# Optimization experiments

Measured on AMD Instinct MI355X. Metric: run time of the kernel, lower is better.

## Reference

```python
import jax, jax.numpy as jnp
import numpy as np

RADIUS = 0.3
NSAMPLE = 16
NPOINT = 256
EPS = 1e-5


def setup_inputs() -> dict:
    key = jax.random.key(0)
    ks = jax.random.split(key, 12)
    B, N, C = 16, 16384, 288
    d = {
        "xyz": jax.random.uniform(ks[0], (B, N, 3), jnp.float32),
        "features": jax.random.normal(ks[1], (B, C, N), jnp.float32),
    }
    cin = [C + 3, C, C]  # use_xyz adds 3 to first SharedMLP width
    for i in range(3):
        d[f"W{i}"] = jax.random.normal(ks[2 + i], (C, cin[i]), jnp.float32) / np.float32(np.sqrt(cin[i]))
        d[f"g{i}"] = jnp.ones((C,), jnp.float32)
        d[f"b{i}"] = jnp.zeros((C,), jnp.float32)
        d[f"m{i}"] = jax.random.normal(ks[5 + i], (C,), jnp.float32) * 0.1
        d[f"v{i}"] = jax.random.uniform(ks[8 + i], (C,), jnp.float32, minval=0.5, maxval=1.5)
    return d


def fps(xyz, npoint):
    """Farthest point sampling. xyz: (B,N,3) -> inds (B,npoint) int32."""
    B, N, _ = xyz.shape
    d0 = jnp.full((B, N), 1e10, xyz.dtype)
    i0 = jnp.zeros((B,), jnp.int32)  # CUDA kernel starts from index 0

    def step(carry, _):
        dist, idx = carry
        cur = jnp.take_along_axis(xyz, idx[:, None, None], axis=1)  # (B,1,3)
        d = jnp.sum((xyz - cur) ** 2, axis=-1)  # (B,N)
        dist = jnp.minimum(dist, d)
        nxt = jnp.argmax(dist, axis=-1).astype(jnp.int32)
        return (dist, nxt), idx

    _, inds = jax.lax.scan(step, (d0, i0), None, length=npoint)
    return inds.T  # (B, npoint)


def ball_query(xyz, new_xyz):
    """xyz: (B,N,3), new_xyz: (B,S,3) -> idx (B,S,NSAMPLE) int32.
    First NSAMPLE in-radius indices; pad with the first found index (CUDA semantics)."""
    N = xyz.shape[1]
    d2 = jnp.sum((new_xyz[:, :, None, :] - xyz[:, None, :, :]) ** 2, axis=-1)  # (B,S,N)
    mask = d2 < RADIUS * RADIUS
    cand = jnp.where(mask, jnp.arange(N, dtype=jnp.int32), jnp.int32(N))
    cand = jnp.sort(cand, axis=-1)[..., :NSAMPLE]
    first = cand[..., :1]
    return jnp.where(cand == N, first, cand)


def _mlp_bn_relu(h, W, g, b, m, v):
    # 1x1 Conv2d (no bias) + BatchNorm (running stats) + ReLU on (B,C,S,K)
    h = jnp.einsum('oc,bcsk->bosk', W, h)
    scale = (g * jax.lax.rsqrt(v + EPS))[:, None, None]
    return jax.nn.relu((h - m[:, None, None]) * scale + b[:, None, None])


def reference(xyz, features, W0, g0, b0, m0, v0, W1, g1, b1, m1, v1, W2, g2, b2, m2, v2):
    inds = fps(xyz, NPOINT)                                   # (B,S)
    new_xyz = jax.vmap(lambda p, i: p[i])(xyz, inds)          # (B,S,3)
    idx = ball_query(xyz, new_xyz)                            # (B,S,K)
    g_xyz = jax.vmap(lambda p, i: p[i])(xyz, idx)             # (B,S,K,3)
    g_xyz = (g_xyz - new_xyz[:, :, None, :]) / RADIUS         # normalize_xyz
    g_feat = jax.vmap(lambda f, i: f[:, i])(features, idx)    # (B,C,S,K)
    h = jnp.concatenate([jnp.transpose(g_xyz, (0, 3, 1, 2)), g_feat], axis=1)  # (B,C+3,S,K)
    for (W, g, b, m, v) in ((W0, g0, b0, m0, v0), (W1, g1, b1, m1, v1), (W2, g2, b2, m2, v2)):
        h = _mlp_bn_relu(h, W, g, b, m, v)
    new_features = jnp.max(h, axis=-1)                        # (B,C,S) max-pool over nsample
    return new_xyz, new_features, inds
```

## Files before the change

kernel.cpp:

```cpp
#include <hip/hip_runtime.h>
#include <hip/hip_bf16.h>
#include <string.h>

#define NPT   16384
#define NBAT  16
#define CH    288
#define SP    256
#define KS    16
#define OFF_FEAT 12288L
#define OFF_IND  1191936L

__device__ __forceinline__ float bfbits(unsigned short u){
  unsigned int x = ((unsigned int)u) << 16; float f; __builtin_memcpy(&f,&x,4); return f;
}
__device__ __forceinline__ float ldf(const void* p, long i, int isb){
  if (isb) return __bfloat162float(((const __hip_bfloat16*)p)[i]);
  return ((const float*)p)[i];
}
__device__ __forceinline__ void sto(void* p, long i, float v, int isb){
  if (isb) ((__hip_bfloat16*)p)[i] = __float2bfloat16(v);
  else     ((float*)p)[i] = v;
}
__device__ __forceinline__ void gload_lds(const void* g, void* l){
  __builtin_amdgcn_global_load_lds((const __attribute__((address_space(1))) void*)g,
      (__attribute__((address_space(3))) void*)l, 16, 0, 0);
}
__device__ __forceinline__ unsigned spread4(unsigned x){
  return (x&1u) | ((x&2u)<<2) | ((x&4u)<<4) | ((x&8u)<<6);
}

typedef __attribute__((ext_vector_type(8))) short bf16x8;
typedef __attribute__((ext_vector_type(4))) float f32x4;
typedef __attribute__((ext_vector_type(2))) float f32x2;

__global__ void detect_k(const void* __restrict__ xyz, int* __restrict__ flag){
  __shared__ float red[256];
  const int t = threadIdx.x;
  const unsigned short* u = (const unsigned short*)xyz;
  float m = 0.f;
  for (int i = t; i < 4096; i += 256){
    float f = fabsf(bfbits(u[i]));
    if (f != f) f = 1e30f;
    m = fmaxf(m, f);
  }
  red[t] = m; __syncthreads();
  for (int s = 128; s; s >>= 1){ if (t < s) red[t] = fmaxf(red[t], red[t+s]); __syncthreads(); }
  if (t == 0) *flag = (red[0] < 2.0f) ? 1 : 0;
}

__global__ __launch_bounds__(256) void cvtxyz_k(const void* __restrict__ xyz,
    const int* __restrict__ flag, float* __restrict__ X, float* __restrict__ Y,
    float* __restrict__ Z, float4* __restrict__ P4){
  const int n = blockIdx.x*256 + threadIdx.x;
  const int isb = *flag;
  float x = ldf(xyz, (long)n*3+0, isb);
  float y = ldf(xyz, (long)n*3+1, isb);
  float z = ldf(xyz, (long)n*3+2, isb);
  X[n] = x; Y[n] = y; Z[n] = z;
  P4[n] = make_float4(x, y, z, 0.f);
}

__global__ __launch_bounds__(256) void cvtw_k(const void* __restrict__ W,
    const void* __restrict__ g, const void* __restrict__ bb,
    const void* __restrict__ m, const void* __restrict__ v,
    const int* __restrict__ flag, __hip_bfloat16* __restrict__ Wbf,
    float* __restrict__ scale, float* __restrict__ shift, int Kin){
  const int isb = *flag;
  const int idx = blockIdx.x*256 + threadIdx.x;
  if (idx < 288*296){
    int o = idx / 296, k = idx - o*296;
    float val = (k < Kin) ? ldf(W, (long)o*Kin + k, isb) : 0.f;
    Wbf[idx] = __float2bfloat16(val);
  }
  if (idx < 288){
    float sc = ldf(g, idx, isb) * rsqrtf(ldf(v, idx, isb) + 1e-5f);
    scale[idx] = sc;
    shift[idx] = ldf(bb, idx, isb) - ldf(m, idx, isb)*sc;
  }
}

__global__ __launch_bounds__(1024) void sort_k(const float* __restrict__ X,
    const float* __restrict__ Y, const float* __restrict__ Z,
    float* __restrict__ X2, float* __restrict__ Y2, float* __restrict__ Z2,
    int* __restrict__ I2){
  __shared__ int hist[4096];
  __shared__ int wtot[16];
  const int b = blockIdx.x, t = threadIdx.x, base = b*NPT;
  for (int j = t; j < 4096; j += 1024) hist[j] = 0;
  __syncthreads();
  int cell[16]; float lx[16], ly[16], lz[16];
  #pragma unroll
  for (int i=0;i<16;i++){
    const int id = t + i*1024;
    float x = X[base+id], y = Y[base+id], z = Z[base+id];
    lx[i]=x; ly[i]=y; lz[i]=z;
    int cx = (int)(x*16.f); cx = cx<0?0:(cx>15?15:cx);
    int cy = (int)(y*16.f); cy = cy<0?0:(cy>15?15:cy);
    int cz = (int)(z*16.f); cz = cz<0?0:(cz>15?15:cz);
    cell[i] = (int)(spread4((unsigned)cx) | (spread4((unsigned)cy)<<1) | (spread4((unsigned)cz)<<2));
    atomicAdd(&hist[cell[i]], 1);
  }
  __syncthreads();
  int s0 = hist[t*4], s1 = hist[t*4+1], s2 = hist[t*4+2], s3 = hist[t*4+3];
  int ls = s0+s1+s2+s3;
  int sc = ls;
  #pragma unroll
  for (int off=1; off<64; off<<=1){
    int o = __shfl_up(sc, off, 64);
    if ((t&63) >= off) sc += o;
  }
  if ((t&63) == 63) wtot[t>>6] = sc;
  __syncthreads();
  int wpre = 0;
  #pragma unroll
  for (int w=0; w<16; w++) wpre += (w < (t>>6)) ? wtot[w] : 0;
  const int ebase = wpre + sc - ls;
  hist[t*4]   = ebase;
  hist[t*4+1] = ebase + s0;
  hist[t*4+2] = ebase + s0 + s1;
  hist[t*4+3] = ebase + s0 + s1 + s2;
  __syncthreads();
  #pragma unroll
  for (int i=0;i<16;i++){
    const int dst = atomicAdd(&hist[cell[i]], 1);
    X2[base+dst] = lx[i]; Y2[base+dst] = ly[i]; Z2[base+dst] = lz[i];
    I2[base+dst] = t + i*1024;
  }
}

__global__ __launch_bounds__(1024) __attribute__((amdgpu_waves_per_eu(4,4)))
void fps_k(const float4* __restrict__ P4,
    const float* __restrict__ X2, const float* __restrict__ Y2,
    const float* __restrict__ Z2, const int* __restrict__ I2,
    const int* __restrict__ flag, float* __restrict__ nxyz, void* __restrict__ dout){
  #pragma clang fp contract(off)
  const int b = blockIdx.x, t = threadIdx.x;
  const int base = b*NPT;
  const int lane = t & 63, wid = t >> 6;
  f32x2 px[8], py[8], pz[8], ds[8];
  unsigned li[16];
  const int p0 = base + wid*1024 + lane;
  #pragma unroll
  for (int j=0;j<8;j++){
    px[j] = (f32x2){X2[p0 + (2*j)*64], X2[p0 + (2*j+1)*64]};
    py[j] = (f32x2){Y2[p0 + (2*j)*64], Y2[p0 + (2*j+1)*64]};
    pz[j] = (f32x2){Z2[p0 + (2*j)*64], Z2[p0 + (2*j+1)*64]};
    li[2*j]   = 16383u - (unsigned)I2[p0 + (2*j)*64];
    li[2*j+1] = 16383u - (unsigned)I2[p0 + (2*j+1)*64];
    ds[j] = (f32x2){1e10f, 1e10f};
  }
  float bxn=px[0].x,bxx=px[0].x,byn=py[0].x,byx=py[0].x,bzn=pz[0].x,bzx=pz[0].x;
  #pragma unroll
  for (int j=0;j<8;j++){
    bxn=fminf(bxn,fminf(px[j].x,px[j].y)); bxx=fmaxf(bxx,fmaxf(px[j].x,px[j].y));
    byn=fminf(byn,fminf(py[j].x,py[j].y)); byx=fmaxf(byx,fmaxf(py[j].x,py[j].y));
    bzn=fminf(bzn,fminf(pz[j].x,pz[j].y)); bzx=fmaxf(bzx,fmaxf(pz[j].x,pz[j].y));
  }
  #pragma unroll
  for (int off=32; off; off>>=1){
    bxn=fminf(bxn,__shfl_xor(bxn,off,64)); bxx=fmaxf(bxx,__shfl_xor(bxx,off,64));
    byn=fminf(byn,__shfl_xor(byn,off,64)); byx=fmaxf(byx,__shfl_xor(byx,off,64));
    bzn=fminf(bzn,__shfl_xor(bzn,off,64)); bzx=fmaxf(bzx,__shfl_xor(bzx,off,64));
  }
  __shared__ unsigned long long slot[2][16];
  __shared__ float ox[SP], oy[SP], oz[SP];
  __shared__ int   oi[SP];
  float4 c4 = P4[base];
  float cx = c4.x, cy = c4.y, cz = c4.z;
  int cur = 0;
  unsigned long long wkey = 0ull;
  float wavemax = 1e30f;
  for (int it=0; it<SP; it++){
    if (t == 0){ ox[it]=cx; oy[it]=cy; oz[it]=cz; oi[it]=cur; }
    float ddx = fmaxf(fmaxf(bxn-cx, cx-bxx), 0.f);
    float ddy = fmaxf(fmaxf(byn-cy, cy-byx), 0.f);
    float ddz = fmaxf(fmaxf(bzn-cz, cz-bzx), 0.f);
    float lb = ddx*ddx + ddy*ddy + ddz*ddz;
    if (!(lb * 0.9999f > wavemax)){
      const f32x2 Cx = {cx,cx}, Cy = {cy,cy}, Cz = {cz,cz};
      unsigned long long best = 0ull;
      #pragma unroll
      for (int j=0;j<8;j++){
        f32x2 dx = px[j]-Cx, dy = py[j]-Cy, dz = pz[j]-Cz;
        f32x2 m0 = dx*dx, m1 = dy*dy, m2 = dz*dz;
        f32x2 d2 = (m0+m1)+m2;
        f32x2 dn = __builtin_elementwise_min(ds[j], d2);
        ds[j] = dn;
        unsigned long long k0 = ((unsigned long long)__float_as_uint(dn.x)<<32)
                              | (unsigned long long)li[2*j];
        unsigned long long k1 = ((unsigned long long)__float_as_uint(dn.y)<<32)
                              | (unsigned long long)li[2*j+1];
        best = (k0 > best) ? k0 : best;
        best = (k1 > best) ? k1 : best;
      }
      #pragma unroll
      for (int off=32; off; off>>=1){
        unsigned long long o = __shfl_xor(best, off, 64);
        best = (o > best) ? o : best;
      }
      wkey = best;
      wavemax = __uint_as_float((unsigned)(best >> 32));
    }
    const int p = it & 1;
    if (lane == 0) slot[p][wid] = wkey;
    __syncthreads();
    unsigned long long g = slot[p][lane & 15];
    #pragma unroll
    for (int m=8; m; m>>=1){
      unsigned long long o = __shfl_xor(g, m, 64);
      g = (o > g) ? o : g;
    }
    cur = 16383 - (int)(unsigned)g;
    cur = __builtin_amdgcn_readfirstlane(cur);
    c4 = P4[base+cur];
    cx = c4.x; cy = c4.y; cz = c4.z;
  }
  __syncthreads();
  if (t < SP){
    const int isb = *flag;
    const long bs = (long)b*SP + t;
    float fx=ox[t], fy=oy[t], fz=oz[t]; int ii=oi[t];
    nxyz[bs*3+0]=fx; nxyz[bs*3+1]=fy; nxyz[bs*3+2]=fz;
    sto(dout, bs*3+0, fx, isb);
    sto(dout, bs*3+1, fy, isb);
    sto(dout, bs*3+2, fz, isb);
    sto(dout, OFF_IND + bs, (float)ii, isb);
  }
}

__global__ __launch_bounds__(256) void ballq_k(const float* __restrict__ X,
    const float* __restrict__ Y, const float* __restrict__ Z,
    const float* __restrict__ nxyz, int* __restrict__ bidx){
  #pragma clang fp contract(off)
  const int gw = (blockIdx.x*256 + threadIdx.x) >> 6;
  const int lane = threadIdx.x & 63;
  const int b = gw >> 8, base = b*NPT;
  const float cx = nxyz[gw*3+0], cy = nxyz[gw*3+1], cz = nxyz[gw*3+2];
  int cnt = 0, first = 0; bool havef = false;
  for (int st = 0; st < NPT && cnt < KS; st += 64){
    const int id = st + lane;
    float dx = X[base+id]-cx, dy = Y[base+id]-cy, dz = Z[base+id]-cz;
    float d2 = dx*dx + dy*dy; d2 = d2 + dz*dz;
    unsigned long long mk = __ballot(d2 <= 0.09f);
    if (mk){
      if (!havef){ first = st + __builtin_ctzll(mk); havef = true; }
      int rank = cnt + __popcll(mk & ((1ull<<lane)-1ull));
      if (((mk>>lane)&1ull) && rank < KS) bidx[gw*KS + rank] = id;
      cnt += __popcll(mk);
    }
  }
  if (cnt < KS && lane >= cnt && lane < KS) bidx[gw*KS + lane] = first;
}

__global__ __launch_bounds__(256) void gather_k(const void* __restrict__ xyz,
    const void* __restrict__ feat, const int* __restrict__ flag,
    const int* __restrict__ bidx, const float* __restrict__ nxyz,
    __hip_bfloat16* __restrict__ h0){
  __shared__ __hip_bfloat16 tile[64*296];
  const int isb = *flag;
  const int t = threadIdx.x, n0 = blockIdx.x*64;
  const int nl = t >> 2, cg = t & 3;
  const int n = n0 + nl, b = n >> 12, s = n >> 4;
  const int id = bidx[n];
  for (int j=0; j<74; j++){
    int c = cg*74 + j;
    float vv = 0.f;
    if (c < 3)       vv = (ldf(xyz, ((long)b*NPT + id)*3 + c, isb) - nxyz[(long)s*3 + c]) / 0.3f;
    else if (c < 291) vv = ldf(feat, ((long)b*CH + (c-3))*(long)NPT + id, isb);
    tile[nl*296 + c] = __float2bfloat16(vv);
  }
  __syncthreads();
  const uint4* src = (const uint4*)tile;
  uint4* dst = (uint4*)((char*)h0 + (long)n0*592);
  for (int j = t; j < 2368; j += 256) dst[j] = src[j];
}

__global__ __launch_bounds__(256, 2) void gemm_k(
    const __hip_bfloat16* __restrict__ A, int astr,
    const __hip_bfloat16* __restrict__ W,
    const float* __restrict__ scale, const float* __restrict__ shift,
    __hip_bfloat16* __restrict__ Out, int ostr,
    int ktiles, int kvalid){
  extern __shared__ char lds[];
  const int t = threadIdx.x, lane = t & 63, wid = t >> 6;
  const int wm = wid & 1, wo = wid >> 1;
  const int bx = blockIdx.x, by = blockIdx.y;
  {
    const char* src = (const char*)(A + (long)bx*128*astr);
    const int chunks = (128*astr*2) >> 10;
    for (int c = wid; c < chunks; c += 4)
      gload_lds(src + c*1024 + lane*16, lds + c*1024);
  }
  f32x4 acc[4][3];
  #pragma unroll
  for (int mf=0; mf<4; mf++)
    #pragma unroll
    for (int of=0; of<3; of++) acc[mf][of] = (f32x4){0.f,0.f,0.f,0.f};

  const int mrow  = wm*64 + (lane & 15);
  const int kg    = (lane >> 4) * 8;
  const int obase = by*96 + wo*48 + (lane & 15);
  __syncthreads();

  for (int kt = 0; kt < ktiles; kt++){
    const int k0 = kt*32 + kg;
    const bool z = (k0 >= kvalid);
    const int k0c = z ? 0 : k0;
    bf16x8 a[4], bf[3];
    #pragma unroll
    for (int mf=0; mf<4; mf++)
      a[mf] = *(const bf16x8*)(lds + ((long)(mrow + mf*16)*astr + k0c)*2);
    if (z){
      bf16x8 zz = {0,0,0,0,0,0,0,0};
      #pragma unroll
      for (int mf=0; mf<4; mf++) a[mf] = zz;
    }
    #pragma unroll
    for (int of=0; of<3; of++)
      bf[of] = *(const bf16x8*)(W + (long)(obase + of*16)*296 + k0c);
    #pragma unroll
    for (int mf=0; mf<4; mf++)
      #pragma unroll
      for (int of=0; of<3; of++)
        acc[mf][of] = __builtin_amdgcn_mfma_f32_16x16x32_bf16(a[mf], bf[of], acc[mf][of], 0, 0, 0);
  }

  float sc[3], sh[3];
  #pragma unroll
  for (int of=0; of<3; of++){ sc[of] = scale[obase + of*16]; sh[of] = shift[obase + of*16]; }
  #pragma unroll
  for (int mf=0; mf<4; mf++)
    #pragma unroll
    for (int of=0; of<3; of++)
      #pragma unroll
      for (int r=0; r<4; r++){
        const long row = (long)bx*128 + wm*64 + mf*16 + (lane>>4)*4 + r;
        const int o = obase + of*16;
        float vv = acc[mf][of][r]*sc[of] + sh[of];
        Out[row*ostr + o] = __float2bfloat16(fmaxf(vv, 0.f));
      }
}

__global__ __launch_bounds__(256) void maxk_k(const __hip_bfloat16* __restrict__ h,
    const int* __restrict__ flag, void* __restrict__ dout){
  __shared__ __hip_bfloat16 tile[128*288];
  const int isb = *flag;
  const int t = threadIdx.x;
  const int b = blockIdx.x >> 5, s0 = (blockIdx.x & 31)*8;
  const long n0 = (long)b*4096 + (long)s0*16;
  {
    const char* src = (const char*)(h + n0*288);
    for (int c = (t>>6); c < 72; c += 4)
      gload_lds(src + c*1024 + (t&63)*16, (char*)tile + c*1024);
  }
  __syncthreads();
  for (int o = t; o < 288; o += 256){
    float mx[8];
    #pragma unroll
    for (int sl=0; sl<8; sl++){
      float m = -1e30f;
      #pragma unroll
      for (int kk=0; kk<16; kk++)
        m = fmaxf(m, __bfloat162float(tile[(sl*16 + kk)*288 + o]));
      mx[sl] = m;
    }
    const long e0 = OFF_FEAT + (long)b*73728 + (long)o*256 + s0;
    if (isb){
      unsigned short u[8];
      #pragma unroll
      for (int sl=0; sl<8; sl++){
        __hip_bfloat16 hb = __float2bfloat16(mx[sl]);
        __builtin_memcpy(&u[sl], &hb, 2);
      }
      uint4 pk; __builtin_memcpy(&pk, u, 16);
      *(uint4*)((__hip_bfloat16*)dout + e0) = pk;
    } else {
      float* fo = (float*)dout + e0;
      *(float4*)fo     = make_float4(mx[0],mx[1],mx[2],mx[3]);
      *(float4*)(fo+4) = make_float4(mx[4],mx[5],mx[6],mx[7]);
    }
  }
}

extern "C" void kernel_launch(void* const* d_in, const int* in_sizes, int n_in,
                              void* d_out, int out_size, void* d_ws, size_t ws_size,
                              hipStream_t stream){
  const void* xyz  = d_in[0];
  const void* feat = d_in[1];
  const void* W0 = d_in[2];  const void* g0 = d_in[3];  const void* b0 = d_in[4];
  const void* m0 = d_in[5];  const void* v0 = d_in[6];
  const void* W1 = d_in[7];  const void* g1 = d_in[8];  const void* b1 = d_in[9];
  const void* m1 = d_in[10]; const void* v1 = d_in[11];
  const void* W2 = d_in[12]; const void* g2 = d_in[13]; const void* b2 = d_in[14];
  const void* m2 = d_in[15]; const void* v2 = d_in[16];

  char* ws = (char*)d_ws;
  int*   flag  = (int*)ws;
  float* sc0   = (float*)(ws + 64);
  float* sh0   = sc0 + 288;
  float* sc1   = sc0 + 576;  float* sh1 = sc0 + 864;
  float* sc2   = sc0 + 1152; float* sh2 = sc0 + 1440;
  __hip_bfloat16* Wb0 = (__hip_bfloat16*)(ws + 7040);
  __hip_bfloat16* Wb1 = Wb0 + 288*296;
  __hip_bfloat16* Wb2 = Wb1 + 288*296;
  float* nxyz = (float*)(ws + 518656);
  int*   bidx = (int*)(ws + 567808);
  float* X    = (float*)(ws + 1048576);
  float* Y    = X + NBAT*NPT;
  float* Z    = Y + NBAT*NPT;
  float4* P4  = (float4*)(ws + 1048576 + 3145728);
  __hip_bfloat16* bufA = (__hip_bfloat16*)(ws + 1048576);
  __hip_bfloat16* bufB = (__hip_bfloat16*)(ws + 1048576 + 38797312);
  float* X2 = (float*)bufB;
  float* Y2 = X2 + NBAT*NPT;
  float* Z2 = Y2 + NBAT*NPT;
  int*   I2 = (int*)(Z2 + NBAT*NPT);

  detect_k<<<1, 256, 0, stream>>>(xyz, flag);
  cvtxyz_k<<<1024, 256, 0, stream>>>(xyz, flag, X, Y, Z, P4);
  cvtw_k<<<333, 256, 0, stream>>>(W0, g0, b0, m0, v0, flag, Wb0, sc0, sh0, 291);
  cvtw_k<<<333, 256, 0, stream>>>(W1, g1, b1, m1, v1, flag, Wb1, sc1, sh1, 288);
  cvtw_k<<<333, 256, 0, stream>>>(W2, g2, b2, m2, v2, flag, Wb2, sc2, sh2, 288);
  sort_k<<<NBAT, 1024, 0, stream>>>(X, Y, Z, X2, Y2, Z2, I2);
  fps_k<<<NBAT, 1024, 0, stream>>>(P4, X2, Y2, Z2, I2, flag, nxyz, d_out);
  ballq_k<<<1024, 256, 0, stream>>>(X, Y, Z, nxyz, bidx);
  gather_k<<<1024, 256, 0, stream>>>(xyz, feat, flag, bidx, nxyz, bufA);
  gemm_k<<<dim3(512,3), 256, 128*296*2, stream>>>(bufA, 296, Wb0, sc0, sh0, bufB, 288, 10, 296);
  gemm_k<<<dim3(512,3), 256, 128*288*2, stream>>>(bufB, 288, Wb1, sc1, sh1, bufA, 296, 9, 288);
  gemm_k<<<dim3(512,3), 256, 128*296*2, stream>>>(bufA, 296, Wb2, sc2, sh2, bufB, 288, 9, 288);
  maxk_k<<<512, 256, 0, stream>>>(bufB, flag, d_out);
}
```

Measured before the change: 1.009 ms.

## Use per-slice bounding-box culling and DPP reductions in FPS loop

Each wave now keeps a bounding box per slot j (eight sub-groups of 128 points), not one box per wave. A ballot decides which slots can still contain the farthest point, and only those slots recompute distances, with cached per-slot best keys reused for the rest. The 64-bit max reductions switch from shfl_xor to DPP row rotations plus readlane, and indices are packed two per register to save VGPRs. This adds per-slot register state and branching in exchange for skipping distance updates and cutting reduction latency on the serial FPS critical path.

New measurement: 934.9 us. -7.4%, faster.

```diff
diff --git a/kernel.cpp b/kernel.cpp
--- a/kernel.cpp
+++ b/kernel.cpp
@@ -32,6 +32,26 @@
 typedef __attribute__((ext_vector_type(8))) short bf16x8;
 typedef __attribute__((ext_vector_type(4))) float f32x4;
 typedef __attribute__((ext_vector_type(2))) float f32x2;
+
+template<int CTRL>
+__device__ __forceinline__ unsigned long long ror_max64(unsigned long long k){
+  int lo2 = __builtin_amdgcn_update_dpp(0, (int)(unsigned)k, CTRL, 0xf, 0xf, false);
+  int hi2 = __builtin_amdgcn_update_dpp(0, (int)(unsigned)(k>>32), CTRL, 0xf, 0xf, false);
+  unsigned long long o = ((unsigned long long)(unsigned)hi2 << 32) | (unsigned)lo2;
+  return o > k ? o : k;
+}
+__device__ __forceinline__ unsigned long long rowmax64(unsigned long long k){
+  k = ror_max64<0x121>(k);
+  k = ror_max64<0x122>(k);
+  k = ror_max64<0x124>(k);
+  k = ror_max64<0x128>(k);
+  return k;
+}
+__device__ __forceinline__ unsigned long long rl64(unsigned long long v, int l){
+  unsigned lo = (unsigned)__builtin_amdgcn_readlane((int)(unsigned)v, l);
+  unsigned hi = (unsigned)__builtin_amdgcn_readlane((int)(unsigned)(v>>32), l);
+  return (((unsigned long long)hi)<<32) | lo;
+}
 
 __global__ void detect_k(const void* __restrict__ xyz, int* __restrict__ flag){
   __shared__ float red[256];
@@ -138,29 +158,34 @@
   const int base = b*NPT;
   const int lane = t & 63, wid = t >> 6;
   f32x2 px[8], py[8], pz[8], ds[8];
-  unsigned li[16];
+  unsigned li2[8];
+  unsigned long long pk[8];
   const int p0 = base + wid*1024 + lane;
   #pragma unroll
   for (int j=0;j<8;j++){
     px[j] = (f32x2){X2[p0 + (2*j)*64], X2[p0 + (2*j+1)*64]};
     py[j] = (f32x2){Y2[p0 + (2*j)*64], Y2[p0 + (2*j+1)*64]};
     pz[j] = (f32x2){Z2[p0 + (2*j)*64], Z2[p0 + (2*j+1)*64]};
-    li[2*j]   = 16383u - (unsigned)I2[p0 + (2*j)*64];
-    li[2*j+1] = 16383u - (unsigned)I2[p0 + (2*j+1)*64];
+    unsigned a = 16383u - (unsigned)I2[p0 + (2*j)*64];
+    unsigned c = 16383u - (unsigned)I2[p0 + (2*j+1)*64];
+    li2[j] = a | (c<<16);
     ds[j] = (f32x2){1e10f, 1e10f};
-  }
-  float bxn=px[0].x,bxx=px[0].x,byn=py[0].x,byx=py[0].x,bzn=pz[0].x,bzx=pz[0].x;
+    pk[j] = 0ull;
+  }
+  float pnx=0.f, pxx=0.f, pny=0.f, pxy=0.f, pnz=0.f, pxz=0.f;
+  const int myp = lane & 7;
   #pragma unroll
   for (int j=0;j<8;j++){
-    bxn=fminf(bxn,fminf(px[j].x,px[j].y)); bxx=fmaxf(bxx,fmaxf(px[j].x,px[j].y));
-    byn=fminf(byn,fminf(py[j].x,py[j].y)); byx=fmaxf(byx,fmaxf(py[j].x,py[j].y));
-    bzn=fminf(bzn,fminf(pz[j].x,pz[j].y)); bzx=fmaxf(bzx,fmaxf(pz[j].x,pz[j].y));
-  }
-  #pragma unroll
-  for (int off=32; off; off>>=1){
-    bxn=fminf(bxn,__shfl_xor(bxn,off,64)); bxx=fmaxf(bxx,__shfl_xor(bxx,off,64));
-    byn=fminf(byn,__shfl_xor(byn,off,64)); byx=fmaxf(byx,__shfl_xor(byx,off,64));
-    bzn=fminf(bzn,__shfl_xor(bzn,off,64)); bzx=fmaxf(bzx,__shfl_xor(bzx,off,64));
+    float nx = fminf(px[j].x,px[j].y), xx = fmaxf(px[j].x,px[j].y);
+    float ny = fminf(py[j].x,py[j].y), xy = fmaxf(py[j].x,py[j].y);
+    float nz = fminf(pz[j].x,pz[j].y), xz = fmaxf(pz[j].x,pz[j].y);
+    #pragma unroll
+    for (int off=32; off; off>>=1){
+      nx = fminf(nx, __shfl_xor(nx, off, 64)); xx = fmaxf(xx, __shfl_xor(xx, off, 64));
+      ny = fminf(ny, __shfl_xor(ny, off, 64)); xy = fmaxf(xy, __shfl_xor(xy, off, 64));
+      nz = fminf(nz, __shfl_xor(nz, off, 64)); xz = fmaxf(xz, __shfl_xor(xz, off, 64));
+    }
+    if (myp == j){ pnx=nx; pxx=xx; pny=ny; pxy=xy; pnz=nz; pxz=xz; }
   }
   __shared__ unsigned long long slot[2][16];
   __shared__ float ox[SP], oy[SP], oz[SP];
@@ -168,48 +193,45 @@
   float4 c4 = P4[base];
   float cx = c4.x, cy = c4.y, cz = c4.z;
   int cur = 0;
-  unsigned long long wkey = 0ull;
+  unsigned long long wk = 0ull;
   float wavemax = 1e30f;
   for (int it=0; it<SP; it++){
     if (t == 0){ ox[it]=cx; oy[it]=cy; oz[it]=cz; oi[it]=cur; }
-    float ddx = fmaxf(fmaxf(bxn-cx, cx-bxx), 0.f);
-    float ddy = fmaxf(fmaxf(byn-cy, cy-byx), 0.f);
-    float ddz = fmaxf(fmaxf(bzn-cz, cz-bzx), 0.f);
-    float lb = ddx*ddx + ddy*ddy + ddz*ddz;
-    if (!(lb * 0.9999f > wavemax)){
+    float ddx = fmaxf(fmaxf(pnx-cx, cx-pxx), 0.f);
+    float ddy = fmaxf(fmaxf(pny-cy, cy-pxy), 0.f);
+    float ddz = fmaxf(fmaxf(pnz-cz, cz-pxz), 0.f);
+    float lb = ddx*ddx + ddy*ddy; lb = lb + ddz*ddz;
+    unsigned mask = (unsigned)__ballot(!(lb * 0.9999f > wavemax)) & 0xffu;
+    mask = (unsigned)__builtin_amdgcn_readfirstlane((int)mask);
+    if (mask){
       const f32x2 Cx = {cx,cx}, Cy = {cy,cy}, Cz = {cz,cz};
-      unsigned long long best = 0ull;
-      #pragma unroll
-      for (int j=0;j<8;j++){
-        f32x2 dx = px[j]-Cx, dy = py[j]-Cy, dz = pz[j]-Cz;
-        f32x2 m0 = dx*dx, m1 = dy*dy, m2 = dz*dz;
-        f32x2 d2 = (m0+m1)+m2;
-        f32x2 dn = __builtin_elementwise_min(ds[j], d2);
-        ds[j] = dn;
-        unsigned long long k0 = ((unsigned long long)__float_as_uint(dn.x)<<32)
-                              | (unsigned long long)li[2*j];
-        unsigned long long k1 = ((unsigned long long)__float_as_uint(dn.y)<<32)
-                              | (unsigned long long)li[2*j+1];
-        best = (k0 > best) ? k0 : best;
-        best = (k1 > best) ? k1 : best;
-      }
-      #pragma unroll
-      for (int off=32; off; off>>=1){
-        unsigned long long o = __shfl_xor(best, off, 64);
-        best = (o > best) ? o : best;
-      }
-      wkey = best;
-      wavemax = __uint_as_float((unsigned)(best >> 32));
+      #define UPD(j) if (mask & (1u<<(j))) { \
+        f32x2 dx = px[j]-Cx, dy = py[j]-Cy, dz = pz[j]-Cz; \
+        f32x2 m0 = dx*dx, m1 = dy*dy, m2 = dz*dz; \
+        f32x2 d2 = (m0+m1)+m2; \
+        f32x2 dn = __builtin_elementwise_min(ds[j], d2); \
+        ds[j] = dn; \
+        unsigned long long k0 = ((unsigned long long)__float_as_uint(dn.x)<<32) | (unsigned long long)(li2[j] & 0xFFFFu); \
+        unsigned long long k1 = ((unsigned long long)__float_as_uint(dn.y)<<32) | (unsigned long long)(li2[j] >> 16); \
+        pk[j] = (k0 > k1) ? k0 : k1; }
+      UPD(0) UPD(1) UPD(2) UPD(3) UPD(4) UPD(5) UPD(6) UPD(7)
+      #undef UPD
+      unsigned long long best = pk[0];
+      #pragma unroll
+      for (int j=1;j<8;j++) best = (pk[j] > best) ? pk[j] : best;
+      best = rowmax64(best);
+      unsigned long long r0 = rl64(best, 0),  r1 = rl64(best, 16);
+      unsigned long long r2 = rl64(best, 32), r3 = rl64(best, 48);
+      unsigned long long a01 = (r0 > r1) ? r0 : r1;
+      unsigned long long a23 = (r2 > r3) ? r2 : r3;
+      wk = (a01 > a23) ? a01 : a23;
+      wavemax = __uint_as_float((unsigned)(wk >> 32));
     }
     const int p = it & 1;
-    if (lane == 0) slot[p][wid] = wkey;
+    if (lane == 0) slot[p][wid] = wk;
     __syncthreads();
     unsigned long long g = slot[p][lane & 15];
-    #pragma unroll
-    for (int m=8; m; m>>=1){
-      unsigned long long o = __shfl_xor(g, m, 64);
-      g = (o > g) ? o : g;
-    }
+    g = rowmax64(g);
     cur = 16383 - (int)(unsigned)g;
     cur = __builtin_amdgcn_readfirstlane(cur);
     c4 = P4[base+cur];
```
